# Kernel optimization log

Measured on AMD Instinct MI355X. Metric: run time of the kernel, lower is better.

## Reference

```python
import jax, jax.numpy as jnp
from jax import lax
import numpy as np

B, T, D, H = 32, 2048, 512, 512


def setup_inputs() -> dict:
    key = jax.random.key(0)
    k1, k2, k3, k4, k5 = jax.random.split(key, 5)
    s = 1.0 / np.sqrt(H)
    return {
        "inputs": jax.random.normal(k1, (B, T, D), dtype=jnp.float32),
        "h_prev": jax.random.normal(k2, (B, H), dtype=jnp.float32),
        # LSTMCell parameters, gate order (i, f, g, o) stacked along first dim
        "W_ih": jax.random.uniform(k3, (4 * H, D), jnp.float32, -s, s),
        "W_hh": jax.random.uniform(k4, (4 * H, H), jnp.float32, -s, s),
        "b": jax.random.uniform(k5, (4 * H,), jnp.float32, -s, s),
    }


def reference(inputs, h_prev, W_ih, W_hh, b):
    # inputs: [B, T, D], h_prev: [B, H]
    batch = inputs.shape[0]
    hid = h_prev.shape[1]
    c_prev = jnp.zeros((batch, hid), dtype=inputs.dtype)
    # Precompute input projections for all timesteps: [T, B, 4H]
    x_proj = jnp.einsum("btd,gd->tbg", inputs, W_ih) + b

    def step(carry, xp_t):
        h, c = carry
        gates = xp_t + h @ W_hh.T  # [B, 4H]
        i, f, g, o = jnp.split(gates, 4, axis=-1)
        i = jax.nn.sigmoid(i)
        f = jax.nn.sigmoid(f)
        g = jnp.tanh(g)
        o = jax.nn.sigmoid(o)
        c_next = f * c + i * g
        h_next = o * jnp.tanh(c_next)
        return (h_next, c_next), None

    (h_last, _), _ = lax.scan(step, (h_prev, c_prev), x_proj)
    return h_last
```

## Files before the change

kernel.cpp:

```cpp
#include <hip/hip_runtime.h>

typedef _Float16 f16;
typedef _Float16 f16x8 __attribute__((ext_vector_type(8)));
typedef float f32x4 __attribute__((ext_vector_type(4)));
typedef unsigned long long u64;
typedef unsigned short u16;
typedef unsigned int u32;

#define NT 2048
#define ND 512
#define NH 512
#define NWG 16
#define SENTW 0xFFFFFFFFFFFFFFFFull
#define SENTH ((u16)0xFFFFu)

__device__ __forceinline__ float sigf(float x)  { return 1.0f / (1.0f + __expf(-x)); }
__device__ __forceinline__ float tanhf_(float x){ return 2.0f / (1.0f + __expf(-2.0f * x)) - 1.0f; }

__device__ __forceinline__ bool has_sent(u64 x) {
  u64 a = x & (x >> 8); a &= (a >> 4); a &= (a >> 2); a &= (a >> 1);
  return (a & 0x0001000100010001ull) != 0ull;
}

__device__ __forceinline__ int frag_idx(int b, int k0) {
  return ((k0 >> 5) * 2 + (b >> 4)) * 64 + ((k0 & 31) >> 3) * 16 + (b & 15);
}

__global__ void lstm_init(const float* __restrict__ hprev, u64* __restrict__ hg) {
  const int g = blockIdx.x * 256 + threadIdx.x;
  const int slot = g >> 12, w = g & 4095;
  u64 v = SENTW;
  if (slot == 0) {
    const int f8 = w >> 1;
    const int b  = ((f8 >> 6) & 1) * 16 + (f8 & 15);
    const int c0 = (f8 >> 7) * 32 + ((f8 >> 4) & 3) * 8 + (w & 1) * 4;
    const float* s = hprev + (size_t)b * NH + c0;
    union { u64 u; f16 h[4]; } pk;
    pk.h[0] = (f16)s[0]; pk.h[1] = (f16)s[1]; pk.h[2] = (f16)s[2]; pk.h[3] = (f16)s[3];
    v = pk.u;
  }
  __hip_atomic_store(hg + g, v, __ATOMIC_RELAXED, __HIP_MEMORY_SCOPE_AGENT);
}

__global__ void __launch_bounds__(256, 1)
lstm_xproj(const float* __restrict__ X, const float* __restrict__ Wih,
           const float* __restrict__ bias, u64* __restrict__ xp) {
  __shared__ __align__(16) f16 x_lds[16384];
  const int tid = threadIdx.x, lane = tid & 63;
  const int wv = tid >> 6, l15 = lane & 15, lg = lane >> 4;
  const int tb = blockIdx.x, cb = blockIdx.y;
  const int colbase = cb * 16 + wv * 4;

  f16x8 wf[16];
#pragma unroll
  for (int kt = 0; kt < 16; ++kt) {
    const float* src = Wih + ((size_t)(l15 & 3) * NH + colbase + (l15 >> 2)) * ND + kt * 32 + lg * 8;
    f32x4 u0 = *(const f32x4*)src, u1 = *(const f32x4*)(src + 4);
    f16x8 w;
    w[0]=(f16)u0[0]; w[1]=(f16)u0[1]; w[2]=(f16)u0[2]; w[3]=(f16)u0[3];
    w[4]=(f16)u1[0]; w[5]=(f16)u1[1]; w[6]=(f16)u1[2]; w[7]=(f16)u1[3];
    wf[kt] = w;
  }
  const int mycol = colbase + lg;
  float bs[4];
#pragma unroll
  for (int q = 0; q < 4; ++q) bs[q] = bias[q * NH + mycol];

  const int gb = tid >> 3, gc0 = (tid & 7) * 64;

  for (int tt = 0; tt < 16; ++tt) {
    const int t = tb * 16 + tt;
    const float* xs = X + ((size_t)gb * NT + t) * ND + gc0;
#pragma unroll
    for (int i = 0; i < 8; ++i) {
      f32x4 v0 = *(const f32x4*)(xs + 8 * i);
      f32x4 v1 = *(const f32x4*)(xs + 8 * i + 4);
      f16x8 h8;
      h8[0]=(f16)v0[0]; h8[1]=(f16)v0[1]; h8[2]=(f16)v0[2]; h8[3]=(f16)v0[3];
      h8[4]=(f16)v1[0]; h8[5]=(f16)v1[1]; h8[6]=(f16)v1[2]; h8[7]=(f16)v1[3];
      *(f16x8*)&x_lds[frag_idx(gb, gc0 + 8 * i) * 8] = h8;
    }
    __syncthreads();

    f32x4 acc0 = {0,0,0,0}, acc1 = {0,0,0,0};
#pragma unroll
    for (int kt = 0; kt < 16; ++kt) {
      f16x8 b0 = *(const f16x8*)&x_lds[((kt * 2 + 0) * 64 + lane) * 8];
      f16x8 b1 = *(const f16x8*)&x_lds[((kt * 2 + 1) * 64 + lane) * 8];
      acc0 = __builtin_amdgcn_mfma_f32_16x16x32_f16(wf[kt], b0, acc0, 0, 0, 0);
      acc1 = __builtin_amdgcn_mfma_f32_16x16x32_f16(wf[kt], b1, acc1, 0, 0, 0);
    }
#pragma unroll
    for (int bh = 0; bh < 2; ++bh) {
      const f32x4& a = bh ? acc1 : acc0;
      union { u64 u; f16 h[4]; } pk;
      pk.h[0] = (f16)(a[0] + bs[0]); pk.h[1] = (f16)(a[1] + bs[1]);
      pk.h[2] = (f16)(a[2] + bs[2]); pk.h[3] = (f16)(a[3] + bs[3]);
      __hip_atomic_store(xp + ((size_t)t * NH + mycol) * 32 + bh * 16 + l15, pk.u,
                         __ATOMIC_RELAXED, __HIP_MEMORY_SCOPE_AGENT);
    }
    __syncthreads();
  }
}

__global__ void __launch_bounds__(256, 1)
lstm_rec(const float* __restrict__ Whh,
         const u64*   __restrict__ xp,
         float* __restrict__ out,
         u64*   __restrict__ hg) {
  __shared__ __align__(16) f16 hbuf[2][16384];

  const int tid = threadIdx.x, lane = tid & 63;
  const int wv = tid >> 6, l15 = lane & 15, lg = lane >> 4;
  const int wgid = blockIdx.x;
  const int colW = wgid * 32 + wv * 8;

  f16x8 wfa[2][16];
#pragma unroll
  for (int a = 0; a < 2; ++a)
#pragma unroll
    for (int kt = 0; kt < 16; ++kt) {
      const float* src = Whh + ((size_t)(l15 & 3) * NH + colW + a * 4 + (l15 >> 2)) * NH + kt * 32 + lg * 8;
      f32x4 u0 = *(const f32x4*)src, u1 = *(const f32x4*)(src + 4);
      f16x8 w;
      w[0]=(f16)u0[0]; w[1]=(f16)u0[1]; w[2]=(f16)u0[2]; w[3]=(f16)u0[3];
      w[4]=(f16)u1[0]; w[5]=(f16)u1[1]; w[6]=(f16)u1[2]; w[7]=(f16)u1[3];
      wfa[a][kt] = w;
    }

  u16* hgh = (u16*)hg;
  int phw[2][2], qaddr[2][2], oaddr[2][2];
#pragma unroll
  for (int a = 0; a < 2; ++a)
#pragma unroll
    for (int bh = 0; bh < 2; ++bh) {
      const int b = bh * 16 + l15, col = colW + a * 4 + lg;
      phw[a][bh]   = ((wgid * 2 + bh) * 64 + wv * 16 + l15) * 8 + a * 4 + lg;
      qaddr[a][bh] = col * 32 + b;
      oaddr[a][bh] = b * NH + col;
    }

  float c[2][2] = {{0.f, 0.f}, {0.f, 0.f}};

  for (int t = 0; t < NT; ++t) {
    const u64* xpt = xp + (size_t)t * 16384;
    u64 xv[2][2];
#pragma unroll
    for (int a = 0; a < 2; ++a)
#pragma unroll
      for (int bh = 0; bh < 2; ++bh) xv[a][bh] = xpt[qaddr[a][bh]];

    {
      u16* rb = hgh + ((size_t)((t + 2) & 3) << 14);
#pragma unroll
      for (int a = 0; a < 2; ++a)
#pragma unroll
        for (int bh = 0; bh < 2; ++bh)
          __hip_atomic_store(rb + phw[a][bh], SENTH, __ATOMIC_RELAXED, __HIP_MEMORY_SCOPE_AGENT);
    }

    u64 g[16];
    {
      const u64* src = hg + ((size_t)(t & 3) << 12) + tid;
#pragma unroll
      for (int i = 0; i < 16; ++i)
        g[i] = __hip_atomic_load(src + 256 * i, __ATOMIC_RELAXED, __HIP_MEMORY_SCOPE_AGENT);
      while (true) {
        u32 bad = 0;
#pragma unroll
        for (int i = 0; i < 16; ++i) if (has_sent(g[i])) bad |= 1u << i;
        if (!__any(bad != 0)) break;
#pragma unroll
        for (int i = 0; i < 16; ++i)
          if (bad & (1u << i))
            g[i] = __hip_atomic_load(src + 256 * i, __ATOMIC_RELAXED, __HIP_MEMORY_SCOPE_AGENT);
      }
    }
    asm volatile("s_waitcnt vmcnt(0)" ::: "memory");

    {
      u64* hb64 = (u64*)hbuf[t & 1];
#pragma unroll
      for (int i = 0; i < 16; ++i)
        hb64[tid + 256 * i] = g[i];
    }
    __syncthreads();

    f32x4 acc[2][2] = {{{0,0,0,0},{0,0,0,0}},{{0,0,0,0},{0,0,0,0}}};
    {
      const f16* hb = hbuf[t & 1];
#pragma unroll
      for (int kt = 0; kt < 16; ++kt) {
        f16x8 b0 = *(const f16x8*)&hb[((kt * 2 + 0) * 64 + lane) * 8];
        f16x8 b1 = *(const f16x8*)&hb[((kt * 2 + 1) * 64 + lane) * 8];
        acc[0][0] = __builtin_amdgcn_mfma_f32_16x16x32_f16(wfa[0][kt], b0, acc[0][0], 0, 0, 0);
        acc[1][0] = __builtin_amdgcn_mfma_f32_16x16x32_f16(wfa[1][kt], b0, acc[1][0], 0, 0, 0);
        acc[0][1] = __builtin_amdgcn_mfma_f32_16x16x32_f16(wfa[0][kt], b1, acc[0][1], 0, 0, 0);
        acc[1][1] = __builtin_amdgcn_mfma_f32_16x16x32_f16(wfa[1][kt], b1, acc[1][1], 0, 0, 0);
      }
    }

    {
      u16* pb = hgh + ((size_t)((t + 1) & 3) << 14);
#pragma unroll
      for (int a = 0; a < 2; ++a)
#pragma unroll
        for (int bh = 0; bh < 2; ++bh) {
          const f16* xg = (const f16*)&xv[a][bh];
          float gi = acc[a][bh][0] + (float)xg[0];
          float gf = acc[a][bh][1] + (float)xg[1];
          float gg = acc[a][bh][2] + (float)xg[2];
          float go = acc[a][bh][3] + (float)xg[3];
          c[a][bh] = sigf(gf) * c[a][bh] + sigf(gi) * tanhf_(gg);
          float hv = sigf(go) * tanhf_(c[a][bh]);
          union { f16 h; u16 u; } cv; cv.h = (f16)hv;
          __hip_atomic_store(pb + phw[a][bh], cv.u, __ATOMIC_RELAXED, __HIP_MEMORY_SCOPE_AGENT);
          if (t == NT - 1) out[oaddr[a][bh]] = hv;
        }
    }
  }
}

extern "C" void kernel_launch(void* const* d_in, const int* in_sizes, int n_in,
                              void* d_out, int out_size, void* d_ws, size_t ws_size,
                              hipStream_t stream) {
  const float* X     = (const float*)d_in[0];
  const float* hprev = (const float*)d_in[1];
  const float* Wih   = (const float*)d_in[2];
  const float* Whh   = (const float*)d_in[3];
  const float* bias  = (const float*)d_in[4];
  float* out = (float*)d_out;

  u64* hg = (u64*)d_ws;
  u64* xp = (u64*)((char*)d_ws + (size_t)(1 << 17));

  hipLaunchKernelGGL(lstm_init, dim3(64), dim3(256), 0, stream, hprev, hg);
  hipLaunchKernelGGL(lstm_xproj, dim3(128, 32), dim3(256), 0, stream, X, Wih, bias, xp);
  hipLaunchKernelGGL(lstm_rec, dim3(NWG), dim3(256), 0, stream, Whh, xp, out, hg);
}
```

Before: 9.111 ms.

## Co-locate recurrent workgroups on one XCC and use sc0 loads/stores for h exchange

The launch grows to 256 workgroups. Each workgroup reads its XCC id and registers with a per-XCC counter, and the first XCC to collect 16 workgroups is elected; all other workgroups exit. The recurrence now runs entirely within one XCC, so the hidden-state exchange can use sc0-scoped global loads and stores, which keeps traffic in that XCC's L2 instead of going to device-coherent memory. A fallback switches to the original agent-scope atomic polling after 256 spin rounds. The risks are the cost of the election, correctness if the scoping assumptions fail, and extra launch overhead from the exiting blocks.

```diff
diff --git a/kernel.cpp b/kernel.cpp
--- a/kernel.cpp
+++ b/kernel.cpp
@@ -26,8 +26,46 @@
   return ((k0 >> 5) * 2 + (b >> 4)) * 64 + ((k0 & 31) >> 3) * 16 + (b & 15);
 }
 
-__global__ void lstm_init(const float* __restrict__ hprev, u64* __restrict__ hg) {
+__device__ __forceinline__ void st_u16_sc0(u16* p, u32 v) {
+  asm volatile("global_store_short %0, %1, off sc0" :: "v"(p), "v"(v) : "memory");
+}
+
+__device__ __forceinline__ void gather16_sc0(const u64* slot, u32 tid, u64* g) {
+  const u32 voff = tid * 8u;
+  asm volatile(
+    "global_load_dwordx2 %0, %16, %17 sc0\n\t"
+    "global_load_dwordx2 %1, %16, %17 offset:2048 sc0\n\t"
+    "global_load_dwordx2 %2, %16, %18 sc0\n\t"
+    "global_load_dwordx2 %3, %16, %18 offset:2048 sc0\n\t"
+    "global_load_dwordx2 %4, %16, %19 sc0\n\t"
+    "global_load_dwordx2 %5, %16, %19 offset:2048 sc0\n\t"
+    "global_load_dwordx2 %6, %16, %20 sc0\n\t"
+    "global_load_dwordx2 %7, %16, %20 offset:2048 sc0\n\t"
+    "global_load_dwordx2 %8, %16, %21 sc0\n\t"
+    "global_load_dwordx2 %9, %16, %21 offset:2048 sc0\n\t"
+    "global_load_dwordx2 %10, %16, %22 sc0\n\t"
+    "global_load_dwordx2 %11, %16, %22 offset:2048 sc0\n\t"
+    "global_load_dwordx2 %12, %16, %23 sc0\n\t"
+    "global_load_dwordx2 %13, %16, %23 offset:2048 sc0\n\t"
+    "global_load_dwordx2 %14, %16, %24 sc0\n\t"
+    "global_load_dwordx2 %15, %16, %24 offset:2048 sc0\n\t"
+    "s_waitcnt vmcnt(0)"
+    : "=&v"(g[0]), "=&v"(g[1]), "=&v"(g[2]), "=&v"(g[3]),
+      "=&v"(g[4]), "=&v"(g[5]), "=&v"(g[6]), "=&v"(g[7]),
+      "=&v"(g[8]), "=&v"(g[9]), "=&v"(g[10]), "=&v"(g[11]),
+      "=&v"(g[12]), "=&v"(g[13]), "=&v"(g[14]), "=&v"(g[15])
+    : "v"(voff),
+      "s"(slot), "s"(slot + 512), "s"(slot + 1024), "s"(slot + 1536),
+      "s"(slot + 2048), "s"(slot + 2560), "s"(slot + 3072), "s"(slot + 3584)
+    : "memory");
+}
+
+__global__ void lstm_init(const float* __restrict__ hprev, u64* __restrict__ hg,
+                          int* __restrict__ ectrl) {
   const int g = blockIdx.x * 256 + threadIdx.x;
+  if (blockIdx.x == 0 && threadIdx.x < 16)
+    __hip_atomic_store(ectrl + threadIdx.x, (threadIdx.x == 8) ? -1 : 0,
+                       __ATOMIC_RELAXED, __HIP_MEMORY_SCOPE_AGENT);
   const int slot = g >> 12, w = g & 4095;
   u64 v = SENTW;
   if (slot == 0) {
@@ -107,12 +145,33 @@
 lstm_rec(const float* __restrict__ Whh,
          const u64*   __restrict__ xp,
          float* __restrict__ out,
-         u64*   __restrict__ hg) {
+         u64*   __restrict__ hg,
+         int*   __restrict__ ectrl) {
   __shared__ __align__(16) f16 hbuf[2][16384];
-
-  const int tid = threadIdx.x, lane = tid & 63;
+  __shared__ int s_wg;
+
+  const int tid = threadIdx.x;
+
+  u32 xcc;
+  asm volatile("s_getreg_b32 %0, hwreg(HW_REG_XCC_ID)" : "=s"(xcc));
+  xcc &= 7;
+  if (tid == 0) {
+    int r = __hip_atomic_fetch_add(ectrl + xcc, 1, __ATOMIC_RELAXED, __HIP_MEMORY_SCOPE_AGENT);
+    if (r == NWG - 1) {
+      int exp = -1;
+      __hip_atomic_compare_exchange_strong(ectrl + 8, &exp, (int)xcc,
+          __ATOMIC_RELAXED, __ATOMIC_RELAXED, __HIP_MEMORY_SCOPE_AGENT);
+    }
+    int w;
+    do { w = __hip_atomic_load(ectrl + 8, __ATOMIC_RELAXED, __HIP_MEMORY_SCOPE_AGENT); } while (w < 0);
+    s_wg = (w == (int)xcc && r < NWG) ? r : -1;
+  }
+  __syncthreads();
+  if (s_wg < 0) return;
+  const int wgid = s_wg;
+
+  const int lane = tid & 63;
   const int wv = tid >> 6, l15 = lane & 15, lg = lane >> 4;
-  const int wgid = blockIdx.x;
   const int colW = wgid * 32 + wv * 8;
 
   f16x8 wfa[2][16];
@@ -141,6 +200,7 @@
     }
 
   float c[2][2] = {{0.f, 0.f}, {0.f, 0.f}};
+  int mode = 0;
 
   for (int t = 0; t < NT; ++t) {
     const u64* xpt = xp + (size_t)t * 16384;
@@ -156,16 +216,28 @@
       for (int a = 0; a < 2; ++a)
 #pragma unroll
         for (int bh = 0; bh < 2; ++bh)
-          __hip_atomic_store(rb + phw[a][bh], SENTH, __ATOMIC_RELAXED, __HIP_MEMORY_SCOPE_AGENT);
+          st_u16_sc0(rb + phw[a][bh], SENTH);
     }
 
     u64 g[16];
-    {
-      const u64* src = hg + ((size_t)(t & 3) << 12) + tid;
+    const u64* slot = hg + ((size_t)(t & 3) << 12);
+    if (mode == 0) {
+      int rounds = 0;
+      for (;;) {
+        gather16_sc0(slot, (u32)tid, g);
+        u32 bad = 0;
+#pragma unroll
+        for (int i = 0; i < 16; ++i) if (has_sent(g[i])) bad |= 1u << i;
+        if (!__any(bad != 0)) break;
+        if (++rounds == 256) { mode = 1; break; }
+      }
+    }
+    if (mode) {
+      const u64* src = slot + tid;
 #pragma unroll
       for (int i = 0; i < 16; ++i)
         g[i] = __hip_atomic_load(src + 256 * i, __ATOMIC_RELAXED, __HIP_MEMORY_SCOPE_AGENT);
-      while (true) {
+      for (;;) {
         u32 bad = 0;
 #pragma unroll
         for (int i = 0; i < 16; ++i) if (has_sent(g[i])) bad |= 1u << i;
@@ -175,8 +247,8 @@
           if (bad & (1u << i))
             g[i] = __hip_atomic_load(src + 256 * i, __ATOMIC_RELAXED, __HIP_MEMORY_SCOPE_AGENT);
       }
-    }
-    asm volatile("s_waitcnt vmcnt(0)" ::: "memory");
+      asm volatile("s_waitcnt vmcnt(0)" ::: "memory");
+    }
 
     {
       u64* hb64 = (u64*)hbuf[t & 1];
@@ -214,7 +286,7 @@
           c[a][bh] = sigf(gf) * c[a][bh] + sigf(gi) * tanhf_(gg);
           float hv = sigf(go) * tanhf_(c[a][bh]);
           union { f16 h; u16 u; } cv; cv.h = (f16)hv;
-          __hip_atomic_store(pb + phw[a][bh], cv.u, __ATOMIC_RELAXED, __HIP_MEMORY_SCOPE_AGENT);
+          st_u16_sc0(pb + phw[a][bh], cv.u);
           if (t == NT - 1) out[oaddr[a][bh]] = hv;
         }
     }
@@ -231,10 +303,11 @@
   const float* bias  = (const float*)d_in[4];
   float* out = (float*)d_out;
 
-  u64* hg = (u64*)d_ws;
-  u64* xp = (u64*)((char*)d_ws + (size_t)(1 << 17));
-
-  hipLaunchKernelGGL(lstm_init, dim3(64), dim3(256), 0, stream, hprev, hg);
+  u64* hg    = (u64*)d_ws;
+  int* ectrl = (int*)((char*)d_ws + (size_t)(1 << 17));
+  u64* xp    = (u64*)((char*)d_ws + (size_t)(1 << 17) + 4096);
+
+  hipLaunchKernelGGL(lstm_init, dim3(64), dim3(256), 0, stream, hprev, hg, ectrl);
   hipLaunchKernelGGL(lstm_xproj, dim3(128, 32), dim3(256), 0, stream, X, Wih, bias, xp);
-  hipLaunchKernelGGL(lstm_rec, dim3(NWG), dim3(256), 0, stream, Whh, xp, out, hg);
-}
+  hipLaunchKernelGGL(lstm_rec, dim3(256), dim3(256), 0, stream, Whh, xp, out, hg, ectrl);
+}
```

Measured after the change: 8.937 ms. No clear change (-1.9%).
